# Kernel tuning notes

Measured on AMD Instinct MI355X. Metric: run time of the kernel, lower is better.

Reference implementation:

```python
import jax, jax.numpy as jnp
import numpy as np
import math

D_MODEL = 1024
NHEAD = 16
HEAD_DIM = D_MODEL // NHEAD
D_FF = 4 * D_MODEL
EPS = 1e-5


def _layer_norm(x, g, b):
    mu = jnp.mean(x, axis=-1, keepdims=True)
    var = jnp.mean(jnp.square(x - mu), axis=-1, keepdims=True)
    return (x - mu) * jax.lax.rsqrt(var + EPS) * g + b


def setup_inputs() -> dict:
    key = jax.random.key(0)
    ks = jax.random.split(key, 12)
    B, N = 2, 2048
    s = 1.0 / math.sqrt(D_MODEL)
    inp = {
        "x": jax.random.normal(ks[0], (B, N, D_MODEL), dtype=jnp.float32),
        "wq": jax.random.normal(ks[1], (D_MODEL, D_MODEL), dtype=jnp.float32) * s,
        "bq": jnp.zeros((D_MODEL,), jnp.float32),
        "wk": jax.random.normal(ks[2], (D_MODEL, D_MODEL), dtype=jnp.float32) * s,
        "bk": jnp.zeros((D_MODEL,), jnp.float32),
        "wv": jax.random.normal(ks[3], (D_MODEL, D_MODEL), dtype=jnp.float32) * s,
        "bv": jnp.zeros((D_MODEL,), jnp.float32),
        "wo": jax.random.normal(ks[4], (D_MODEL, D_MODEL), dtype=jnp.float32) * s,
        "bo": jnp.zeros((D_MODEL,), jnp.float32),
        "ln1_g": jnp.ones((D_MODEL,), jnp.float32),
        "ln1_b": jnp.zeros((D_MODEL,), jnp.float32),
        "ln2_g": jnp.ones((D_MODEL,), jnp.float32),
        "ln2_b": jnp.zeros((D_MODEL,), jnp.float32),
        "w1": jax.random.normal(ks[5], (D_MODEL, D_FF), dtype=jnp.float32) * s,
        "b1": jnp.zeros((D_FF,), jnp.float32),
        "w2": jax.random.normal(ks[6], (D_FF, D_MODEL), dtype=jnp.float32) * (1.0 / math.sqrt(D_FF)),
        "b2": jnp.zeros((D_MODEL,), jnp.float32),
    }
    return inp


def reference(x, wq, bq, wk, bk, wv, bv, wo, bo, ln1_g, ln1_b, ln2_g, ln2_b, w1, b1, w2, b2):
    B, N, _ = x.shape
    normed = _layer_norm(x, ln1_g, ln1_b)
    # projections -> [B, H, N, Dh]
    q = (normed @ wq + bq).reshape(B, N, NHEAD, HEAD_DIM).transpose(0, 2, 1, 3)
    k = (normed @ wk + bk).reshape(B, N, NHEAD, HEAD_DIM).transpose(0, 2, 1, 3)
    v = (normed @ wv + bv).reshape(B, N, NHEAD, HEAD_DIM).transpose(0, 2, 1, 3)
    raw_scores = jnp.einsum("bhqd,bhkd->bhqk", q, k) / math.sqrt(HEAD_DIM)
    attn_probs = jax.nn.sigmoid(raw_scores)
    attn_out = jnp.einsum("bhqk,bhkd->bhqd", attn_probs, v) / math.sqrt(N)
    attn_out = attn_out.transpose(0, 2, 1, 3).reshape(B, N, D_MODEL)
    x = x + (attn_out @ wo + bo)  # dropout is identity in eval
    normed2 = _layer_norm(x, ln2_g, ln2_b)
    ff = jax.nn.gelu(normed2 @ w1 + b1, approximate=False) @ w2 + b2
    x = x + ff
    return (x, attn_probs)
```

## Files before the change

### kernel.cpp

```cpp
#include <hip/hip_runtime.h>
#include <hip/hip_bf16.h>
#include <math.h>

#define DMODEL 1024
#define NSEQ   2048
#define NBATCH 2
#define NHEADS 16
#define DHEAD  64
#define DFF    4096
#define MROWS  (NBATCH*NSEQ)
#define QKVLD  3072

typedef __attribute__((ext_vector_type(8))) short bf16x8;
typedef __attribute__((ext_vector_type(4))) float f32x4;

static __device__ __forceinline__ ushort f2b(float f) {
    return __builtin_bit_cast(ushort, (__bf16)f);
}

static __device__ __forceinline__ f32x4 mfma16(bf16x8 a, bf16x8 b, f32x4 c) {
    return __builtin_amdgcn_mfma_f32_16x16x32_bf16(a, b, c, 0, 0, 0);
}

static __device__ __forceinline__ void gload_lds16(const void* g, void* lds) {
    __builtin_amdgcn_global_load_lds((const __attribute__((address_space(1))) void*)g,
                                     (__attribute__((address_space(3))) void*)lds,
                                     16, 0, 0);
}

static __device__ __forceinline__ void softbar() {
    __builtin_amdgcn_sched_barrier(0);
    asm volatile("s_waitcnt lgkmcnt(0)" ::: "memory");
    __builtin_amdgcn_s_barrier();
    __builtin_amdgcn_sched_barrier(0);
}

static __device__ __forceinline__ void cast_tile(const float* __restrict__ W,
                                                 ushort* __restrict__ Wt,
                                                 int K, int Nn, int bx, int by, int t)
{
    const int n  = bx * 64 + (t & 63);
    const int k0 = by * 16 + (t >> 6) * 4;
    ushort tmp[4];
#pragma unroll
    for (int i = 0; i < 4; ++i) tmp[i] = f2b(W[(long)(k0 + i) * Nn + n]);
    *(uint2*)(Wt + (long)n * K + k0) = *(const uint2*)tmp;
}

__global__ __launch_bounds__(256) void prep(const float* __restrict__ wq,
                                            const float* __restrict__ wk,
                                            const float* __restrict__ wv,
                                            const float* __restrict__ wo,
                                            const float* __restrict__ w1,
                                            const float* __restrict__ w2,
                                            const float* __restrict__ bq,
                                            const float* __restrict__ bk,
                                            const float* __restrict__ bv,
                                            const float* __restrict__ x,
                                            const float* __restrict__ ln1g,
                                            const float* __restrict__ ln1b,
                                            ushort* __restrict__ wqkv_t,
                                            ushort* __restrict__ wo_t,
                                            ushort* __restrict__ w1_t,
                                            ushort* __restrict__ w2_t,
                                            float* __restrict__ bqkv,
                                            ushort* __restrict__ normed)
{
    __shared__ float red[4];
    const int id  = blockIdx.x;
    const int tid = threadIdx.x;

    if (id < 1024) {
        cast_tile(wq, wqkv_t, 1024, 1024, id & 15, id >> 4, tid);
    } else if (id < 2048) {
        const int i2 = id - 1024;
        cast_tile(wk, wqkv_t + 1024 * 1024, 1024, 1024, i2 & 15, i2 >> 4, tid);
    } else if (id < 3072) {
        const int i2 = id - 2048;
        cast_tile(wv, wqkv_t + 2048 * 1024, 1024, 1024, i2 & 15, i2 >> 4, tid);
    } else if (id < 4096) {
        const int i2 = id - 3072;
        cast_tile(wo, wo_t, 1024, 1024, i2 & 15, i2 >> 4, tid);
    } else if (id < 8192) {
        const int i2 = id - 4096;
        cast_tile(w1, w1_t, 1024, 4096, i2 & 63, i2 >> 6, tid);
    } else if (id < 12288) {
        const int i2 = id - 8192;
        cast_tile(w2, w2_t, 4096, 1024, i2 & 15, i2 >> 4, tid);
    } else if (id < 12304) {
        const int t = (id - 12288) * 256 + tid;
        float v = 0.0f;
        if (t < 1024)      v = bq[t];
        else if (t < 2048) v = bk[t - 1024];
        else if (t < 3072) v = bv[t - 2048];
        bqkv[t] = v;
    } else {
        const int row = id - 12304;
        const float4 v = ((const float4*)(x + (long)row * DMODEL))[tid];
        float s = v.x + v.y + v.z + v.w;
#pragma unroll
        for (int o = 32; o; o >>= 1) s += __shfl_down(s, o, 64);
        if ((tid & 63) == 0) red[tid >> 6] = s;
        __syncthreads();
        const float mu = (red[0] + red[1] + red[2] + red[3]) * (1.0f / DMODEL);
        __syncthreads();
        const float d0 = v.x - mu, d1 = v.y - mu, d2 = v.z - mu, d3 = v.w - mu;
        float s2 = d0*d0 + d1*d1 + d2*d2 + d3*d3;
#pragma unroll
        for (int o = 32; o; o >>= 1) s2 += __shfl_down(s2, o, 64);
        if ((tid & 63) == 0) red[tid >> 6] = s2;
        __syncthreads();
        const float inv = rsqrtf((red[0] + red[1] + red[2] + red[3]) * (1.0f / DMODEL) + 1e-5f);
        const float4 gg = ((const float4*)ln1g)[tid];
        const float4 bv4 = ((const float4*)ln1b)[tid];
        ushort4 o4;
        o4.x = f2b(d0 * inv * gg.x + bv4.x);
        o4.y = f2b(d1 * inv * gg.y + bv4.y);
        o4.z = f2b(d2 * inv * gg.z + bv4.z);
        o4.w = f2b(d3 * inv * gg.w + bv4.w);
        ((ushort4*)(normed + (long)row * DMODEL))[tid] = o4;
    }
}

__global__ __launch_bounds__(256) void ln_kernel(const float* __restrict__ x,
                                                 const float* __restrict__ g,
                                                 const float* __restrict__ bb,
                                                 ushort* __restrict__ out)
{
    const int row = blockIdx.x;
    const int tid = threadIdx.x;
    const float4 v = ((const float4*)(x + (long)row * DMODEL))[tid];
    float s = v.x + v.y + v.z + v.w;
#pragma unroll
    for (int o = 32; o; o >>= 1) s += __shfl_down(s, o, 64);
    __shared__ float red[4];
    if ((tid & 63) == 0) red[tid >> 6] = s;
    __syncthreads();
    const float mu = (red[0] + red[1] + red[2] + red[3]) * (1.0f / DMODEL);
    __syncthreads();
    const float d0 = v.x - mu, d1 = v.y - mu, d2 = v.z - mu, d3 = v.w - mu;
    float s2 = d0*d0 + d1*d1 + d2*d2 + d3*d3;
#pragma unroll
    for (int o = 32; o; o >>= 1) s2 += __shfl_down(s2, o, 64);
    if ((tid & 63) == 0) red[tid >> 6] = s2;
    __syncthreads();
    const float inv = rsqrtf((red[0] + red[1] + red[2] + red[3]) * (1.0f / DMODEL) + 1e-5f);
    const float4 gg = ((const float4*)g)[tid];
    const float4 bv = ((const float4*)bb)[tid];
    ushort4 o4;
    o4.x = f2b(d0 * inv * gg.x + bv.x);
    o4.y = f2b(d1 * inv * gg.y + bv.y);
    o4.z = f2b(d2 * inv * gg.z + bv.z);
    o4.w = f2b(d3 * inv * gg.w + bv.w);
    ((ushort4*)(out + (long)row * DMODEL))[tid] = o4;
}

template<bool GELU>
__global__ __launch_bounds__(512, 2) void gemm8(const ushort* __restrict__ A, int lda,
                                                const ushort* __restrict__ Bt, int ldb,
                                                const float* __restrict__ bias,
                                                ushort* __restrict__ C, int ldc, int K)
{
    extern __shared__ char smem[];
    const int tid  = threadIdx.x;
    const int lane = tid & 63;
    const int w    = tid >> 6;
    const int wm   = w >> 2;
    const int wn   = w & 3;
    const long row0 = (long)blockIdx.x * 256;
    const long col0 = (long)blockIdx.y * 256;

    const int srow = tid >> 2;
    const int scol = (((tid & 3) ^ ((srow >> 1) & 3))) * 8;
    const ushort* Ag = A  + (row0 + srow) * (long)lda + scol;
    const ushort* Bg = Bt + (col0 + srow) * (long)ldb + scol;

#define STAGE_A8(buf, k0)                                                                  \
    do {                                                                                   \
        gload_lds16(Ag + (k0),                  smem + ((buf) << 14) + w * 1024);          \
        gload_lds16(Ag + 128 * (long)lda + (k0), smem + ((buf) << 14) + 8192 + w * 1024);  \
    } while (0)
#define STAGE_B8(buf, k0)                                                                  \
    do {                                                                                   \
        gload_lds16(Bg + (k0),                  smem + 65536 + ((buf) << 14) + w * 1024);  \
        gload_lds16(Bg + 128 * (long)ldb + (k0), smem + 65536 + ((buf) << 14) + 8192 + w * 1024); \
    } while (0)

    const f32x4 zero = {0.f, 0.f, 0.f, 0.f};
    f32x4 acc[8][4];
#pragma unroll
    for (int m = 0; m < 8; ++m)
#pragma unroll
        for (int j = 0; j < 4; ++j) acc[m][j] = zero;

    const int NT = K >> 5;
    STAGE_A8(0, 0);  STAGE_B8(0, 0);
    STAGE_A8(1, 32); STAGE_B8(1, 32);

    const int mrow = lane & 15;
    const int xsl  = (((lane >> 4) ^ ((mrow >> 1) & 3))) * 8;
    const int abase = (wm * 128 + mrow) * 32 + xsl;
    const int bbase = (wn * 64  + mrow) * 32 + xsl;

    for (int t = 0; t < NT; ++t) {
        if (t == NT - 1) asm volatile("s_waitcnt vmcnt(0)" ::: "memory");
        else             asm volatile("s_waitcnt vmcnt(4)" ::: "memory");
        __builtin_amdgcn_sched_barrier(0);
        __builtin_amdgcn_s_barrier();
        __builtin_amdgcn_sched_barrier(0);

        const ushort* Abase = (const ushort*)(smem + ((t & 3) << 14));
        const ushort* Bbase = (const ushort*)(smem + 65536 + ((t & 3) << 14));

        bf16x8 bfr[4], afr[4];
#pragma unroll
        for (int ni = 0; ni < 4; ++ni)
            bfr[ni] = *(const bf16x8*)&Bbase[bbase + ni * 512];
#pragma unroll
        for (int mi = 0; mi < 4; ++mi)
            afr[mi] = *(const bf16x8*)&Abase[abase + mi * 512];
        if (t + 2 < NT) STAGE_A8((t + 2) & 3, (t + 2) * 32);
        __builtin_amdgcn_s_setprio(1);
#pragma unroll
        for (int mi = 0; mi < 4; ++mi)
#pragma unroll
            for (int ni = 0; ni < 4; ++ni)
                acc[mi][ni] = mfma16(afr[mi], bfr[ni], acc[mi][ni]);
        __builtin_amdgcn_s_setprio(0);

#pragma unroll
        for (int mi = 0; mi < 4; ++mi)
            afr[mi] = *(const bf16x8*)&Abase[abase + (mi + 4) * 512];
        if (t + 2 < NT) STAGE_B8((t + 2) & 3, (t + 2) * 32);
        __builtin_amdgcn_s_setprio(1);
#pragma unroll
        for (int mi = 0; mi < 4; ++mi)
#pragma unroll
            for (int ni = 0; ni < 4; ++ni)
                acc[mi + 4][ni] = mfma16(afr[mi], bfr[ni], acc[mi + 4][ni]);
        __builtin_amdgcn_s_setprio(0);
    }
#undef STAGE_A8
#undef STAGE_B8

#pragma unroll
    for (int ni = 0; ni < 4; ++ni) {
        const int colg = (int)col0 + wn * 64 + ni * 16 + (lane & 15);
        const float bcol = bias[colg];
#pragma unroll
        for (int mi = 0; mi < 8; ++mi) {
#pragma unroll
            for (int r = 0; r < 4; ++r) {
                const long rowg = row0 + wm * 128 + mi * 16 + (lane >> 4) * 4 + r;
                float vv = acc[mi][ni][r] + bcol;
                if (GELU) vv = 0.5f * vv * (1.0f + erff(vv * 0.70710678118f));
                C[rowg * ldc + colg] = f2b(vv);
            }
        }
    }
}

template<bool OUTF32, bool GELU, bool RES, bool NTST>
__global__ __launch_bounds__(512, 2) void gemm4s(const ushort* __restrict__ A, int lda,
                                                 const ushort* __restrict__ Bt, int ldb,
                                                 const float* __restrict__ bias,
                                                 const float* __restrict__ res,
                                                 void* __restrict__ Cout,
                                                 int Nn, int K)
{
    extern __shared__ char smem[];
    const int tid  = threadIdx.x;
    const int lane = tid & 63;
    const int g    = tid >> 8;
    const int tg   = tid & 255;
    const int w4   = tg >> 6;
    const int wm   = w4 >> 1, wn = w4 & 1;
    const long row0 = (long)blockIdx.x * 128;
    const long col0 = (long)blockIdx.y * 128;
    const int mrow = lane & 15;
    const int xsl  = (((lane >> 4) ^ ((mrow >> 1) & 3))) * 8;

    const int srow = tg >> 2;
    const int soff = (((tg & 3) ^ ((srow >> 1) & 3))) * 8;
    const int kb   = g * (K >> 1);
    const ushort* Ag = A  + (row0 + srow) * (long)lda + kb + soff;
    const ushort* Bg = Bt + (col0 + srow) * (long)ldb + kb + soff;
    char* Als = smem + g * 32768;
    char* Bls = smem + 65536 + g * 32768;

#define STAGE4S(buf, k0)                                                          \
    do {                                                                          \
        gload_lds16(Ag + (k0),                  Als + ((buf) << 13) + w4 * 1024); \
        gload_lds16(Ag + 64 * (long)lda + (k0), Als + ((buf) << 13) + 4096 + w4 * 1024); \
        gload_lds16(Bg + (k0),                  Bls + ((buf) << 13) + w4 * 1024); \
        gload_lds16(Bg + 64 * (long)ldb + (k0), Bls + ((buf) << 13) + 4096 + w4 * 1024); \
    } while (0)

    const f32x4 zero = {0.f, 0.f, 0.f, 0.f};
    f32x4 acc[4][4];
#pragma unroll
    for (int m = 0; m < 4; ++m)
#pragma unroll
        for (int j = 0; j < 4; ++j) acc[m][j] = zero;

    const int NT2 = K >> 6;
    STAGE4S(0, 0);
    STAGE4S(1, 32);
    STAGE4S(2, 64);

    const int abase = (wm * 64 + mrow) * 32 + xsl;
    const int bbase = (wn * 64 + mrow) * 32 + xsl;

    for (int t = 0; t < NT2; ++t) {
        if      (t >= NT2 - 1) asm volatile("s_waitcnt vmcnt(0)" ::: "memory");
        else if (t == NT2 - 2) asm volatile("s_waitcnt vmcnt(4)" ::: "memory");
        else                   asm volatile("s_waitcnt vmcnt(8)" ::: "memory");
        __builtin_amdgcn_sched_barrier(0);
        __builtin_amdgcn_s_barrier();
        __builtin_amdgcn_sched_barrier(0);

        if (t + 3 < NT2) STAGE4S((t + 3) & 3, (t + 3) * 32);

        const ushort* Abase = (const ushort*)(Als + ((t & 3) << 13));
        const ushort* Bbase = (const ushort*)(Bls + ((t & 3) << 13));
        bf16x8 af[4], bfv[4];
#pragma unroll
        for (int m = 0; m < 4; ++m)
            af[m] = *(const bf16x8*)&Abase[abase + m * 512];
#pragma unroll
        for (int j = 0; j < 4; ++j)
            bfv[j] = *(const bf16x8*)&Bbase[bbase + j * 512];
        __builtin_amdgcn_s_setprio(1);
#pragma unroll
        for (int m = 0; m < 4; ++m)
#pragma unroll
            for (int j = 0; j < 4; ++j)
                acc[m][j] = mfma16(af[m], bfv[j], acc[m][j]);
        __builtin_amdgcn_s_setprio(0);
    }
#undef STAGE4S

    __syncthreads();
    float* xch = (float*)smem;
    if (g == 1) {
#pragma unroll
        for (int m = 0; m < 4; ++m)
#pragma unroll
            for (int j = 0; j < 4; ++j)
#pragma unroll
                for (int r = 0; r < 4; ++r)
                    xch[(m * 16 + j * 4 + r) * 256 + tg] = acc[m][j][r];
    }
    __syncthreads();
    if (g == 0) {
#pragma unroll
        for (int j = 0; j < 4; ++j) {
            const int colg  = (int)col0 + wn * 64 + j * 16 + mrow;
            const float bcol = bias[colg];
#pragma unroll
            for (int m = 0; m < 4; ++m) {
#pragma unroll
                for (int r = 0; r < 4; ++r) {
                    const long rowg = row0 + wm * 64 + m * 16 + (lane >> 4) * 4 + r;
                    float vv = acc[m][j][r] + xch[(m * 16 + j * 4 + r) * 256 + tg] + bcol;
                    if (RES)   vv += res[rowg * Nn + colg];
                    if (GELU)  vv = 0.5f * vv * (1.0f + erff(vv * 0.70710678118f));
                    if (OUTF32) {
                        if (NTST) __builtin_nontemporal_store(vv, (float*)Cout + rowg * Nn + colg);
                        else      ((float*)Cout)[rowg * Nn + colg] = vv;
                    } else {
                        ((ushort*)Cout)[rowg * Nn + colg] = f2b(vv);
                    }
                }
            }
        }
    }
}

__global__ __launch_bounds__(256) void transpose_v(const ushort* __restrict__ v,
                                                   ushort* __restrict__ vt)
{
    __shared__ ushort t[64][72];
    const int nb = blockIdx.x, bh = blockIdx.y, b = bh >> 4;
    const int hcol = (bh & 15) * DHEAD;
    const int tid  = threadIdx.x;
    const int rrow = tid >> 3;
    const int cch  = (tid & 7) * 8;
#pragma unroll
    for (int r = 0; r < 2; ++r) {
        const int nr = rrow + r * 32;
        *(uint4*)&t[nr][cch] =
            *(const uint4*)(v + ((long)(b * NSEQ + nb * 64 + nr)) * QKVLD + hcol + cch);
    }
    __syncthreads();
#pragma unroll
    for (int r = 0; r < 2; ++r) {
        const int d = rrow + r * 32;
        ushort tmp[8];
#pragma unroll
        for (int i = 0; i < 8; ++i) tmp[i] = t[cch + i][d];
        *(uint4*)(vt + ((long)bh * DHEAD + d) * NSEQ + nb * 64 + cch) = *(const uint4*)tmp;
    }
}

__global__ __launch_bounds__(256) void attn_kernel(const ushort* __restrict__ qkv,
                                                   const ushort* __restrict__ vt,
                                                   float* __restrict__ probs,
                                                   ushort* __restrict__ ao)
{
    __shared__ ushort Ks[64][72];
    __shared__ ushort Vs[64][72];
    __shared__ __align__(16) float Pf[4][16][68];
    const int tid  = threadIdx.x;
    const int lane = tid & 63;
    const int w    = tid >> 6;
    const int qb   = blockIdx.x;
    const int bh   = blockIdx.y;
    const int b    = bh >> 4;
    const int q0   = qb * 64 + w * 16;
    const int mrow = lane & 15;
    const int kof  = (lane >> 4) * 8;
    const int hcol = (bh & 15) * DHEAD;
    const int NT   = NSEQ / 64;

    bf16x8 aq0, aq1;
    {
        const ushort* qp = qkv + ((long)(b * NSEQ + q0 + mrow)) * QKVLD + hcol;
        aq0 = *(const bf16x8*)(qp + kof);
        aq1 = *(const bf16x8*)(qp + 32 + kof);
    }

    const f32x4 zero = {0.f, 0.f, 0.f, 0.f};
    f32x4 acco[4];
#pragma unroll
    for (int dj = 0; dj < 4; ++dj) acco[dj] = zero;

    const int srow = tid >> 3;
    const int sch  = (tid & 7) * 8;
    const ushort* km = qkv + 1024;

    uint4 kr0, kr1, vr0, vr1;
#define LOADT(kt)                                                                          \
    do {                                                                                   \
        kr0 = *(const uint4*)(km + ((long)(b * NSEQ + (kt) * 64 + srow)) * QKVLD + hcol + sch);       \
        kr1 = *(const uint4*)(km + ((long)(b * NSEQ + (kt) * 64 + srow + 32)) * QKVLD + hcol + sch);  \
        vr0 = *(const uint4*)(vt + ((long)bh * DHEAD + srow) * NSEQ + (kt) * 64 + sch);               \
        vr1 = *(const uint4*)(vt + ((long)bh * DHEAD + srow + 32) * NSEQ + (kt) * 64 + sch);          \
    } while (0)

    LOADT(0);

    for (int kt = 0; kt < NT; ++kt) {
        *(uint4*)&Ks[srow][sch]      = kr0;
        *(uint4*)&Ks[srow + 32][sch] = kr1;
        *(uint4*)&Vs[srow][sch]      = vr0;
        *(uint4*)&Vs[srow + 32][sch] = vr1;
        softbar();
        if (kt + 1 < NT) LOADT(kt + 1);

        f32x4 s[4];
#pragma unroll
        for (int j = 0; j < 4; ++j) s[j] = zero;
#pragma unroll
        for (int j = 0; j < 4; ++j) {
            bf16x8 b0 = *(const bf16x8*)&Ks[j * 16 + mrow][kof];
            bf16x8 b1 = *(const bf16x8*)&Ks[j * 16 + mrow][32 + kof];
            s[j] = mfma16(aq0, b0, s[j]);
            s[j] = mfma16(aq1, b1, s[j]);
        }

#pragma unroll
        for (int j = 0; j < 4; ++j) {
#pragma unroll
            for (int r = 0; r < 4; ++r) {
                const int rr = (lane >> 4) * 4 + r;
                const float e  = __expf(-0.125f * s[j][r]);
                const float pv = __builtin_amdgcn_rcpf(1.0f + e);
                Pf[w][rr][j * 16 + mrow] = pv;
            }
        }

        const long pbase = ((long)(bh * NSEQ + q0)) * NSEQ + kt * 64;
#pragma unroll
        for (int i = 0; i < 4; ++i) {
            const int rr = (lane >> 4) + 4 * i;
            const f32x4 pv4 = *(const f32x4*)&Pf[w][rr][mrow * 4];
            __builtin_nontemporal_store(pv4, (f32x4*)(probs + pbase + (long)rr * NSEQ + mrow * 4));
        }

#pragma unroll
        for (int ks = 0; ks < 2; ++ks) {
            const f32x4 f0 = *(const f32x4*)&Pf[w][mrow][ks * 32 + kof];
            const f32x4 f1 = *(const f32x4*)&Pf[w][mrow][ks * 32 + kof + 4];
            bf16x8 ap;
            ap[0] = (short)f2b(f0[0]); ap[1] = (short)f2b(f0[1]);
            ap[2] = (short)f2b(f0[2]); ap[3] = (short)f2b(f0[3]);
            ap[4] = (short)f2b(f1[0]); ap[5] = (short)f2b(f1[1]);
            ap[6] = (short)f2b(f1[2]); ap[7] = (short)f2b(f1[3]);
#pragma unroll
            for (int dj = 0; dj < 4; ++dj) {
                bf16x8 bv = *(const bf16x8*)&Vs[dj * 16 + mrow][ks * 32 + kof];
                acco[dj] = mfma16(ap, bv, acco[dj]);
            }
        }
        softbar();
    }
#undef LOADT

    const float sc = rsqrtf((float)NSEQ);
#pragma unroll
    for (int dj = 0; dj < 4; ++dj)
#pragma unroll
        for (int r = 0; r < 4; ++r) {
            const int rr = (lane >> 4) * 4 + r;
            ao[((long)(b * NSEQ + q0 + rr)) * DMODEL + hcol + dj * 16 + mrow] =
                f2b(acco[dj][r] * sc);
        }
}

extern "C" void kernel_launch(void* const* d_in, const int* in_sizes, int n_in,
                              void* d_out, int out_size, void* d_ws, size_t ws_size,
                              hipStream_t stream) {
    (void)in_sizes; (void)n_in; (void)out_size;
    const float* x    = (const float*)d_in[0];
    const float* wq   = (const float*)d_in[1];
    const float* bq   = (const float*)d_in[2];
    const float* wk   = (const float*)d_in[3];
    const float* bk   = (const float*)d_in[4];
    const float* wv   = (const float*)d_in[5];
    const float* bv   = (const float*)d_in[6];
    const float* wo   = (const float*)d_in[7];
    const float* bo   = (const float*)d_in[8];
    const float* ln1g = (const float*)d_in[9];
    const float* ln1b = (const float*)d_in[10];
    const float* ln2g = (const float*)d_in[11];
    const float* ln2b = (const float*)d_in[12];
    const float* w1   = (const float*)d_in[13];
    const float* b1   = (const float*)d_in[14];
    const float* w2   = (const float*)d_in[15];
    const float* b2   = (const float*)d_in[16];

    char* ws = (char*)d_ws;
    const size_t MB = 1u << 20;
    ushort* wqkv_t  = (ushort*)(ws + 0 * MB);
    ushort* wo_t    = (ushort*)(ws + 6 * MB);
    ushort* w1_t    = (ushort*)(ws + 8 * MB);
    ushort* w2_t    = (ushort*)(ws + 16 * MB);
    float*  bqkv    = (float*) (ws + 24 * MB);
    ushort* normed  = (ushort*)(ws + 25 * MB);
    ushort* qkvbuf  = (ushort*)(ws + 33 * MB);
    ushort* vtb     = (ushort*)(ws + 57 * MB);
    ushort* attn_o  = (ushort*)(ws + 65 * MB);
    float*  x1      = (float*) (ws + 41 * MB);
    ushort* normed2 = (ushort*)(ws + 25 * MB);
    ushort* hbuf    = (ushort*)(ws + 57 * MB);
    const float* bzero = bqkv + 3072;
    const bool fullff = (ws_size >= 90 * MB);

    float* xout  = (float*)d_out;
    float* probs = xout + (size_t)MROWS * DMODEL;

    prep<<<16400, 256, 0, stream>>>(wq, wk, wv, wo, w1, w2, bq, bk, bv,
                                    x, ln1g, ln1b,
                                    wqkv_t, wo_t, w1_t, w2_t, bqkv, normed);

    gemm8<false><<<dim3(16, 12), 512, 128 * 1024, stream>>>(
        normed, DMODEL, wqkv_t, DMODEL, bqkv, qkvbuf, QKVLD, DMODEL);

    transpose_v<<<dim3(NSEQ / 64, NBATCH * NHEADS), 256, 0, stream>>>(qkvbuf + 2048, vtb);

    attn_kernel<<<dim3(NSEQ / 64, NBATCH * NHEADS), 256, 0, stream>>>(
        qkvbuf, vtb, probs, attn_o);

    gemm4s<true, false, true, false><<<dim3(32, 8), 512, 128 * 1024, stream>>>(
        attn_o, DMODEL, wo_t, DMODEL, bo, x, x1, DMODEL, DMODEL);

    ln_kernel<<<MROWS, 256, 0, stream>>>(x1, ln2g, ln2b, normed2);

    if (fullff) {
        gemm8<true><<<dim3(16, 16), 512, 128 * 1024, stream>>>(
            normed2, DMODEL, w1_t, DMODEL, b1, hbuf, DFF, DMODEL);
        gemm4s<true, false, true, true><<<dim3(32, 8), 512, 128 * 1024, stream>>>(
            hbuf, DFF, w2_t, DFF, b2, x1, xout, DMODEL, DFF);
    } else {
        gemm8<true><<<dim3(16, 8), 512, 128 * 1024, stream>>>(
            normed2, DMODEL, w1_t, DMODEL, b1, hbuf, 2048, DMODEL);
        gemm4s<true, false, true, false><<<dim3(32, 8), 512, 128 * 1024, stream>>>(
            hbuf, 2048, w2_t, DFF, b2, x1, xout, DMODEL, 2048);
        gemm8<true><<<dim3(16, 8), 512, 128 * 1024, stream>>>(
            normed2, DMODEL, w1_t + 2048 * 1024, DMODEL, b1 + 2048, hbuf, 2048, DMODEL);
        gemm4s<true, false, true, true><<<dim3(32, 8), 512, 128 * 1024, stream>>>(
            hbuf, 2048, w2_t + 2048, DFF, bzero, xout, xout, DMODEL, 2048);
    }
}
```

Before: 325.0 us.

## Load K and V fragments directly from global memory, dropping LDS staging and barriers

The attention kernel no longer stages K and V tiles through shared memory with block-wide barriers. Each wave now loads its MFMA operand fragments for K (prefetched one tile ahead) and V straight from global memory into registers. This removes the LDS writes and reads and the two barriers per iteration. In exchange, each of the four waves fetches the same K/V data separately, which raises global/L2 traffic, and the V loads are issued in the same iteration they are used, with less latency hiding.

```diff
diff --git a/kernel.cpp b/kernel.cpp
--- a/kernel.cpp
+++ b/kernel.cpp
@@ -26,13 +26,6 @@
     __builtin_amdgcn_global_load_lds((const __attribute__((address_space(1))) void*)g,
                                      (__attribute__((address_space(3))) void*)lds,
                                      16, 0, 0);
-}
-
-static __device__ __forceinline__ void softbar() {
-    __builtin_amdgcn_sched_barrier(0);
-    asm volatile("s_waitcnt lgkmcnt(0)" ::: "memory");
-    __builtin_amdgcn_s_barrier();
-    __builtin_amdgcn_sched_barrier(0);
 }
 
 static __device__ __forceinline__ void cast_tile(const float* __restrict__ W,
@@ -408,8 +401,6 @@
                                                    float* __restrict__ probs,
                                                    ushort* __restrict__ ao)
 {
-    __shared__ ushort Ks[64][72];
-    __shared__ ushort Vs[64][72];
     __shared__ __align__(16) float Pf[4][16][68];
     const int tid  = threadIdx.x;
     const int lane = tid & 63;
@@ -435,38 +426,42 @@
 #pragma unroll
     for (int dj = 0; dj < 4; ++dj) acco[dj] = zero;
 
-    const int srow = tid >> 3;
-    const int sch  = (tid & 7) * 8;
-    const ushort* km = qkv + 1024;
-
-    uint4 kr0, kr1, vr0, vr1;
-#define LOADT(kt)                                                                          \
-    do {                                                                                   \
-        kr0 = *(const uint4*)(km + ((long)(b * NSEQ + (kt) * 64 + srow)) * QKVLD + hcol + sch);       \
-        kr1 = *(const uint4*)(km + ((long)(b * NSEQ + (kt) * 64 + srow + 32)) * QKVLD + hcol + sch);  \
-        vr0 = *(const uint4*)(vt + ((long)bh * DHEAD + srow) * NSEQ + (kt) * 64 + sch);               \
-        vr1 = *(const uint4*)(vt + ((long)bh * DHEAD + srow + 32) * NSEQ + (kt) * 64 + sch);          \
-    } while (0)
-
-    LOADT(0);
+    const ushort* kbase = qkv + 1024 + (long)(b * NSEQ) * QKVLD + hcol;
+    const ushort* vbase = vt + ((long)bh * DHEAD) * NSEQ;
+
+    bf16x8 kb0[4], kb1[4];
+#pragma unroll
+    for (int j = 0; j < 4; ++j) {
+        const ushort* kp = kbase + (long)(j * 16 + mrow) * QKVLD;
+        kb0[j] = *(const bf16x8*)(kp + kof);
+        kb1[j] = *(const bf16x8*)(kp + 32 + kof);
+    }
 
     for (int kt = 0; kt < NT; ++kt) {
-        *(uint4*)&Ks[srow][sch]      = kr0;
-        *(uint4*)&Ks[srow + 32][sch] = kr1;
-        *(uint4*)&Vs[srow][sch]      = vr0;
-        *(uint4*)&Vs[srow + 32][sch] = vr1;
-        softbar();
-        if (kt + 1 < NT) LOADT(kt + 1);
+        bf16x8 vb[2][4];
+#pragma unroll
+        for (int ks = 0; ks < 2; ++ks)
+#pragma unroll
+            for (int dj = 0; dj < 4; ++dj)
+                vb[ks][dj] = *(const bf16x8*)(vbase + (long)(dj * 16 + mrow) * NSEQ
+                                              + kt * 64 + ks * 32 + kof);
 
         f32x4 s[4];
 #pragma unroll
         for (int j = 0; j < 4; ++j) s[j] = zero;
 #pragma unroll
         for (int j = 0; j < 4; ++j) {
-            bf16x8 b0 = *(const bf16x8*)&Ks[j * 16 + mrow][kof];
-            bf16x8 b1 = *(const bf16x8*)&Ks[j * 16 + mrow][32 + kof];
-            s[j] = mfma16(aq0, b0, s[j]);
-            s[j] = mfma16(aq1, b1, s[j]);
+            s[j] = mfma16(aq0, kb0[j], s[j]);
+            s[j] = mfma16(aq1, kb1[j], s[j]);
+        }
+
+        if (kt + 1 < NT) {
+#pragma unroll
+            for (int j = 0; j < 4; ++j) {
+                const ushort* kp = kbase + (long)((kt + 1) * 64 + j * 16 + mrow) * QKVLD;
+                kb0[j] = *(const bf16x8*)(kp + kof);
+                kb1[j] = *(const bf16x8*)(kp + 32 + kof);
+            }
         }
 
 #pragma unroll
@@ -498,14 +493,10 @@
             ap[4] = (short)f2b(f1[0]); ap[5] = (short)f2b(f1[1]);
             ap[6] = (short)f2b(f1[2]); ap[7] = (short)f2b(f1[3]);
 #pragma unroll
-            for (int dj = 0; dj < 4; ++dj) {
-                bf16x8 bv = *(const bf16x8*)&Vs[dj * 16 + mrow][ks * 32 + kof];
-                acco[dj] = mfma16(ap, bv, acco[dj]);
-            }
-        }
-        softbar();
-    }
-#undef LOADT
+            for (int dj = 0; dj < 4; ++dj)
+                acco[dj] = mfma16(ap, vb[ks][dj], acco[dj]);
+        }
+    }
 
     const float sc = rsqrtf((float)NSEQ);
 #pragma unroll
```

Measured after the change: 436.8 us. 34.4% more time.
